# Kernel optimization log

Hardware: AMD Instinct MI355X
Metric: run time of the kernel (lower is better)

## Reference

```python
import jax, jax.numpy as jnp
import numpy as np

B, V, H, W = 8, 2, 1024, 1024
N = 131072
TH_MIN, TH_MAX = 0.0, 500.0
ALPHA = 0.5


def _make_extrinsics():
    # Random small-rotation camera-to-world poses (invertible 4x4), fixed seed.
    rng = np.random.default_rng(0)
    E = np.tile(np.eye(4, dtype=np.float32), (B, V, 1, 1))
    for bi in range(B):
        for vi in range(V):
            ang = rng.uniform(-0.15, 0.15)
            ax = rng.normal(size=3)
            ax = ax / np.linalg.norm(ax)
            K = np.array([[0.0, -ax[2], ax[1]], [ax[2], 0.0, -ax[0]], [-ax[1], ax[0], 0.0]])
            R = np.eye(3) + np.sin(ang) * K + (1.0 - np.cos(ang)) * (K @ K)
            E[bi, vi, :3, :3] = R.astype(np.float32)
            E[bi, vi, :3, 3] = (rng.normal(size=3) * 0.5).astype(np.float32)
    return jnp.asarray(E)


def setup_inputs():
    key = jax.random.key(0)
    k0, k1, k2, k3, k4 = jax.random.split(key, 5)
    scale = jnp.array([W - 1.0, H - 1.0], jnp.float32)
    mkpts0 = jax.random.uniform(k0, (N, 2), dtype=jnp.float32) * scale
    mkpts1 = jax.random.uniform(k1, (N, 2), dtype=jnp.float32) * scale
    mconf = jax.random.uniform(k2, (N,), jnp.float32, 0.2, 1.0)
    mbids = jnp.sort(jax.random.randint(k3, (N,), 0, B, dtype=jnp.int32))
    intr = jnp.tile(jnp.array([[1.0, 0.0, 0.5], [0.0, 1.0, 0.5], [0.0, 0.0, 1.0]], jnp.float32), (B, V, 1, 1))
    extr = _make_extrinsics()
    disps = jax.random.uniform(k4, (V * B, 1, H, W), jnp.float32, 0.01, 1.0)
    return {"mkpts0": mkpts0, "mkpts1": mkpts1, "mconf": mconf, "mbids": mbids,
            "intrinsics": intr, "extrinsics": extr, "fullres_disps": disps}


def _forward(mkpts0, mkpts1, mconf, mbids, intrinsics, extrinsics, fullres_disps):
    b, v = intrinsics.shape[:2]
    _, _, h, w = fullres_disps.shape
    # intr0[0,:]*=w ; intr0[1,:]*=h  (normalized -> pixel intrinsics)
    row_scale = jnp.array([float(w), float(h), 1.0], intrinsics.dtype)[None, None, :, None]
    intr = intrinsics * row_scale                                    # (b,v,3,3)
    extr_inv = jnp.linalg.inv(extrinsics)                            # (b,v,4,4)
    proj = jnp.einsum('bvij,bvjk->bvik', intr, extr_inv[:, :, :3, :])  # (b,v,3,4)

    # --- per-keypoint DLT triangulation (vectorized over all N matches) ---
    P = proj[mbids]                                                  # (N,v,3,4)
    pts2 = jnp.stack([mkpts0, mkpts1], axis=1)                       # (N,v,2)
    # rows: conf*(x*P[2]-P[0]), conf*(y*P[2]-P[1])
    A = P[:, :, 2:3, :] * pts2[..., None] - P[:, :, :2, :]           # (N,v,2,4)
    A = A * mconf[:, None, None, None]
    A = A.reshape(-1, 2 * v, 4)                                      # (N,4,4)
    _, _, vh = jnp.linalg.svd(A, full_matrices=False)
    hom = vh[:, -1, :]                                               # last right singular vector
    pts_world = hom[:, :3] / hom[:, 3:4]                             # (N,3)

    # transform into each camera frame: pc_transform(pts, extr.inverse())
    pw_h = jnp.concatenate([pts_world, jnp.ones_like(pts_world[:, :1])], axis=-1)
    pts_cam = jnp.einsum('nvij,nj->nvi', extr_inv[mbids], pw_h)[..., :3]  # (N,v,3)
    z = pts_cam[..., 2]                                              # (N,v)
    valid = jnp.all((z > TH_MIN) & (z < TH_MAX), axis=1)             # (N,)

    # --- near/far over valid matched depths per (scene, view) ---
    zmin = jnp.where(valid[:, None], z, jnp.inf)
    zmax = jnp.where(valid[:, None], z, -jnp.inf)
    near = jax.ops.segment_min(zmin, mbids, num_segments=b)          # (b,v)
    far = jax.ops.segment_max(zmax, mbids, num_segments=b)
    has = jax.ops.segment_max(valid.astype(jnp.float32), mbids, num_segments=b)
    flag = jnp.broadcast_to(has[:, None], (b, v))                    # (b,v)
    near = jnp.where(flag > 0, near, 0.0)
    far = jnp.where(flag > 0, far, 500.0)

    # --- fusion_mkpt_costvolum: scatter 1/z into the cost-volume disparities ---
    disps = fullres_disps.reshape(v, b, h, w)                        # '(v b) 1 h w'
    mk_x = jnp.clip(jnp.stack([mkpts0[:, 0], mkpts1[:, 0]], 1).astype(jnp.int32), 0, w - 1)  # (N,v)
    mk_y = jnp.clip(jnp.stack([mkpts0[:, 1], mkpts1[:, 1]], 1).astype(jnp.int32), 0, h - 1)
    mk_z = 1.0 / z                                                   # matched disparity (N,v)
    view_idx = jnp.broadcast_to(jnp.arange(v, dtype=jnp.int32)[None, :], mk_x.shape)
    bids2 = jnp.broadcast_to(mbids[:, None], mk_x.shape)
    cost = disps[view_idx, bids2, mk_y, mk_x]                        # gather existing disparity
    val = ALPHA * mk_z + (1.0 - ALPHA) * cost                        # alpha-weighted fusion
    val = jnp.where(valid[:, None], val, cost)                       # masked-out matches: no-op write
    disps = disps.at[view_idx, bids2, mk_y, mk_x].set(val)
    fused = disps.reshape(v * b, 1, h, w)
    return fused, near, far, flag


def reference(mkpts0, mkpts1, mconf, mbids, intrinsics, extrinsics, fullres_disps):
    return _forward(mkpts0, mkpts1, mconf, mbids, intrinsics, extrinsics, fullres_disps)
```

## Files before the change

kernel.cpp:

```cpp
#include <hip/hip_runtime.h>
#include <math.h>

#define BB 8
#define VV 2
#define HH 1024
#define WW 1024
#define NPTS 131072
#define IMG (HH*WW)
#define FUSED (VV*BB*IMG)

#define NSOLVE (NPTS/256)
#define F4TOT  (FUSED/4)

#define PER_CP   4
#define NC_K1    2048
#define COPY_K1  (NC_K1*256*PER_CP)
#define NC_K2    2048

#define NC_FB    (F4TOT/(256*PER_CP))

typedef float f32x4 __attribute__((ext_vector_type(4)));

#define OFF_VAL  0u
#define OFF_PIX  (8u*NPTS)
#define OFF_RED  (16u*NPTS)
#define OFF_WIN  (OFF_RED + 0x20000u)
#define WS_NEED  ((size_t)OFF_WIN + 4ull*(size_t)FUSED)

__device__ __forceinline__ int clampi(int v, int lo, int hi) {
    return v < lo ? lo : (v > hi ? hi : v);
}

__device__ __forceinline__ void prep_one(int t, const float* __restrict__ intr,
                                         const float* __restrict__ extr, double* sD) {
    const float* E = extr + t * 16;
    double R[3][3], tr[3];
#pragma unroll
    for (int i = 0; i < 3; i++) {
#pragma unroll
        for (int j = 0; j < 3; j++) R[i][j] = (double)E[i * 4 + j];
        tr[i] = (double)E[i * 4 + 3];
    }
    double inv[3][4];
#pragma unroll
    for (int i = 0; i < 3; i++) {
#pragma unroll
        for (int j = 0; j < 3; j++) inv[i][j] = R[j][i];
        inv[i][3] = -(R[0][i] * tr[0] + R[1][i] * tr[1] + R[2][i] * tr[2]);
    }
    const float* K = intr + t * 9;
    double rs[3] = {(double)WW, (double)HH, 1.0};
#pragma unroll
    for (int i = 0; i < 3; i++)
#pragma unroll
        for (int k = 0; k < 4; k++) {
            double s = 0.0;
#pragma unroll
            for (int j = 0; j < 3; j++) s += (double)K[i * 3 + j] * rs[i] * inv[j][k];
            sD[t * 12 + i * 4 + k] = s;
        }
#pragma unroll
    for (int k = 0; k < 4; k++) sD[192 + t * 4 + k] = inv[2][k];
}

__device__ __forceinline__ void copy_chunk(const f32x4* __restrict__ src,
                                           f32x4* __restrict__ dst,
                                           int base, int blk, int t) {
    int s = base + blk * (256 * PER_CP);
#pragma unroll
    for (int k = 0; k < PER_CP; k++) {
        int i = s + k * 256 + t;
        f32x4 v = src[i];
        __builtin_nontemporal_store(v, &dst[i]);
    }
}

template <int DEDUP>
__global__ __launch_bounds__(256) void mega_kernel(
        const f32x4* __restrict__ src, f32x4* __restrict__ dst,
        const float2* __restrict__ mk0, const float2* __restrict__ mk1,
        const int* __restrict__ mbids,
        const float* __restrict__ intr, const float* __restrict__ extr,
        const float* __restrict__ disps,
        float* __restrict__ out, char* __restrict__ ws) {
    int b = blockIdx.x, t = threadIdx.x;

    if (b >= NSOLVE) {
        copy_chunk(src, dst, 0, b - NSOLVE, t);
        return;
    }

    __shared__ double sD[256];
    __shared__ int nearB[16], farB[16], hasB[8];
    if (t < 16) {
        prep_one(t, intr, extr, sD);
        nearB[t] = 0x7F800000;
        farB[t]  = 0;
        if (t < 8) hasB[t] = 0;
    }
    __syncthreads();

    int n = b * 256 + t;
    float* valarr = (float*)(ws + OFF_VAL);
    int*   pixarr = (int*)(ws + OFF_PIX);
    int*   winner = (int*)(ws + OFF_WIN);

    int bid = mbids[n];
    float2 q0 = mk0[n], q1 = mk1[n];
    float xf[2] = {q0.x, q1.x};
    float yf[2] = {q0.y, q1.y};

    double M[4][4];
#pragma unroll
    for (int i = 0; i < 4; i++)
#pragma unroll
        for (int j = 0; j < 4; j++) M[i][j] = 0.0;
#pragma unroll
    for (int v = 0; v < 2; v++) {
        const double* P = sD + (bid * VV + v) * 12;
        double xx = (double)xf[v], yy = (double)yf[v];
        double r0[4], r1[4];
#pragma unroll
        for (int j = 0; j < 4; j++) {
            r0[j] = xx * P[8 + j] - P[j];
            r1[j] = yy * P[8 + j] - P[4 + j];
        }
#pragma unroll
        for (int i = 0; i < 4; i++)
#pragma unroll
            for (int j = 0; j < 4; j++) M[i][j] += r0[i] * r0[j] + r1[i] * r1[j];
    }

    double Vm[4][4] = {{1, 0, 0, 0}, {0, 1, 0, 0}, {0, 0, 1, 0}, {0, 0, 0, 1}};
    for (int sweep = 0; sweep < 8; ++sweep) {
        double off = fabs(M[0][1]) + fabs(M[0][2]) + fabs(M[0][3]) +
                     fabs(M[1][2]) + fabs(M[1][3]) + fabs(M[2][3]);
        double dia = fabs(M[0][0]) + fabs(M[1][1]) + fabs(M[2][2]) + fabs(M[3][3]);
        if (off <= 1e-13 * dia) break;
#pragma unroll
        for (int p = 0; p < 3; p++) {
#pragma unroll
            for (int q = p + 1; q < 4; q++) {
                double apq = M[p][q];
                if (fabs(apq) < 1e-300) continue;
                double tau = (M[q][q] - M[p][p]) / (2.0 * apq);
                double rt  = sqrt(1.0 + tau * tau);
                double t_  = (tau >= 0.0) ? 1.0 / (tau + rt) : 1.0 / (tau - rt);
                double c = 1.0 / sqrt(1.0 + t_ * t_);
                double s = t_ * c;
#pragma unroll
                for (int k = 0; k < 4; k++) {
                    double mp = M[k][p], mq = M[k][q];
                    M[k][p] = c * mp - s * mq;
                    M[k][q] = s * mp + c * mq;
                }
#pragma unroll
                for (int k = 0; k < 4; k++) {
                    double mp = M[p][k], mq = M[q][k];
                    M[p][k] = c * mp - s * mq;
                    M[q][k] = s * mp + c * mq;
                }
#pragma unroll
                for (int k = 0; k < 4; k++) {
                    double vp = Vm[k][p], vq = Vm[k][q];
                    Vm[k][p] = c * vp - s * vq;
                    Vm[k][q] = s * vp + c * vq;
                }
            }
        }
    }
    int jmin = 0; double dmin = M[0][0];
    if (M[1][1] < dmin) { dmin = M[1][1]; jmin = 1; }
    if (M[2][2] < dmin) { dmin = M[2][2]; jmin = 2; }
    if (M[3][3] < dmin) { dmin = M[3][3]; jmin = 3; }

    double ev[4];
#pragma unroll
    for (int i = 0; i < 4; i++) {
        double a01 = (jmin == 0) ? Vm[i][0] : Vm[i][1];
        double a23 = (jmin == 2) ? Vm[i][2] : Vm[i][3];
        ev[i] = (jmin < 2) ? a01 : a23;
    }
    double iw  = 1.0 / ev[3];
    double pwx = ev[0] * iw, pwy = ev[1] * iw, pwz = ev[2] * iw;

    double z[2];
#pragma unroll
    for (int v = 0; v < 2; v++) {
        const double* e = sD + 192 + (bid * VV + v) * 4;
        z[v] = e[0] * pwx + e[1] * pwy + e[2] * pwz + e[3];
    }
    bool valid = (z[0] > 0.0) && (z[0] < 500.0) && (z[1] > 0.0) && (z[1] < 500.0);

    unsigned long long vb = __ballot(valid);
    int bidFirst = __shfl(bid, 0);
    int bidLast  = __shfl(bid, 63);
    if (bidFirst == bidLast) {
        if (vb != 0ULL) {
            float zn[2], zf[2];
#pragma unroll
            for (int v = 0; v < 2; v++) {
                zn[v] = valid ? (float)z[v] : INFINITY;
                zf[v] = valid ? (float)z[v] : -1.0f;
            }
#pragma unroll
            for (int off = 32; off > 0; off >>= 1) {
#pragma unroll
                for (int v = 0; v < 2; v++) {
                    zn[v] = fminf(zn[v], __shfl_down(zn[v], off));
                    zf[v] = fmaxf(zf[v], __shfl_down(zf[v], off));
                }
            }
            if ((t & 63) == 0) {
#pragma unroll
                for (int v = 0; v < 2; v++) {
                    atomicMin(&nearB[bid * VV + v], __float_as_int(zn[v]));
                    atomicMax(&farB[bid * VV + v],  __float_as_int(zf[v]));
                }
                atomicOr(&hasB[bid], 1);
            }
        }
    } else if (valid) {
#pragma unroll
        for (int v = 0; v < 2; v++) {
            int fb = __float_as_int((float)z[v]);
            atomicMin(&nearB[bid * VV + v], fb);
            atomicMax(&farB[bid * VV + v],  fb);
        }
        atomicOr(&hasB[bid], 1);
    }

#pragma unroll
    for (int v = 0; v < 2; v++) {
        int xi = clampi((int)xf[v], 0, WW - 1);
        int yi = clampi((int)yf[v], 0, HH - 1);
        int pix = (v * BB + bid) * IMG + yi * WW + xi;
        float cost = disps[pix];
        if (DEDUP) {
            winner[pix] = 0;
            valarr[2 * n + v] = valid ? (float)(0.5 * (1.0 / z[v]) + 0.5 * (double)cost)
                                      : 0.0f;
            pixarr[2 * n + v] = pix;
        } else {
            float val = valid ? (float)(0.5 * (1.0 / z[v]) + 0.5 * (double)cost) : cost;
            out[pix] = val;
        }
    }

    __syncthreads();
    int* red = (int*)(ws + OFF_RED) + b * 40;
    if (t < 16) {
        red[t]      = nearB[t];
        red[16 + t] = farB[t];
        if (t < 8) red[32 + t] = hasB[t];
    }
}

__device__ __forceinline__ void reduce_nearfar(const char* __restrict__ ws,
                                               float* __restrict__ out) {
    __shared__ int redLds[40];
    int t = threadIdx.x;
    const int* red = (const int*)(ws + OFF_RED);
    int w = t >> 6, lane = t & 63;
    for (int c = w; c < 40; c += 4) {
        int acc = (c < 16) ? 0x7F800000 : 0;
        for (int s = lane; s < NSOLVE; s += 64) {
            int vv = red[s * 40 + c];
            acc = (c < 16) ? min(acc, vv) : (c < 32 ? max(acc, vv) : (acc | vv));
        }
#pragma unroll
        for (int off = 32; off > 0; off >>= 1) {
            int o = __shfl_down(acc, off);
            acc = (c < 16) ? min(acc, o) : (c < 32 ? max(acc, o) : (acc | o));
        }
        if (lane == 0) redLds[c] = acc;
    }
    __syncthreads();
    if (t < 16) {
        int hv = redLds[32 + (t >> 1)];
        out[FUSED + t]               = hv ? __int_as_float(redLds[t])      : 0.0f;
        out[FUSED + BB * VV + t]     = hv ? __int_as_float(redLds[16 + t]) : 500.0f;
        out[FUSED + 2 * BB * VV + t] = hv ? 1.0f : 0.0f;
    }
}

__global__ __launch_bounds__(256) void vote_copy_kernel(
        const f32x4* __restrict__ src, f32x4* __restrict__ dst,
        char* __restrict__ ws, float* __restrict__ out) {
    int b = blockIdx.x, t = threadIdx.x;
    copy_chunk(src, dst, COPY_K1, b, t);
    if (b < NSOLVE) {
        int gid = b * 256 + t;
        const int2* pix2 = (const int2*)(ws + OFF_PIX);
        int* winner = (int*)(ws + OFF_WIN);
        int2 p = pix2[gid];
        atomicMax(winner + p.x, 2 * gid + 1);
        atomicMax(winner + p.y, 2 * gid + 2);
    } else if (b == NSOLVE) {
        reduce_nearfar(ws, out);
    }
}

__global__ __launch_bounds__(256) void resolve_kernel(float* __restrict__ out,
                                                      const char* __restrict__ ws) {
    int gid = blockIdx.x * 256 + threadIdx.x;
    const int2*   pix2 = (const int2*)(ws + OFF_PIX);
    const float2* val2 = (const float2*)(ws + OFF_VAL);
    const int*    winner = (const int*)(ws + OFF_WIN);
    int2 p = pix2[gid];
    float2 v = val2[gid];
    if (v.x > 0.0f && winner[p.x] == 2 * gid + 1) out[p.x] = v.x;
    if (v.y > 0.0f && winner[p.y] == 2 * gid + 2) out[p.y] = v.y;
}

__global__ __launch_bounds__(256) void reduce_kernel(float* __restrict__ out,
                                                     const char* __restrict__ ws) {
    reduce_nearfar(ws, out);
}

extern "C" void kernel_launch(void* const* d_in, const int* in_sizes, int n_in,
                              void* d_out, int out_size, void* d_ws, size_t ws_size,
                              hipStream_t stream) {
    const float* mk0   = (const float*)d_in[0];
    const float* mk1   = (const float*)d_in[1];
    const int*   mbids = (const int*)d_in[3];
    const float* intr  = (const float*)d_in[4];
    const float* extr  = (const float*)d_in[5];
    const float* disps = (const float*)d_in[6];
    float* out = (float*)d_out;
    char*  ws  = (char*)d_ws;

    bool dedup = (ws_size >= WS_NEED);

    if (dedup) {
        mega_kernel<1><<<dim3(NSOLVE + NC_K1), 256, 0, stream>>>(
            (const f32x4*)disps, (f32x4*)out, (const float2*)mk0, (const float2*)mk1,
            mbids, intr, extr, disps, out, ws);
        vote_copy_kernel<<<NC_K2, 256, 0, stream>>>(
            (const f32x4*)disps, (f32x4*)out, ws, out);
        resolve_kernel<<<NSOLVE, 256, 0, stream>>>(out, ws);
    } else {
        mega_kernel<0><<<dim3(NSOLVE + NC_FB), 256, 0, stream>>>(
            (const f32x4*)disps, (f32x4*)out, (const float2*)mk0, (const float2*)mk1,
            mbids, intr, extr, disps, out, ws);
        reduce_kernel<<<1, 256, 0, stream>>>(out, ws);
    }
}
```

Baseline: 186.7 us.

## Run Jacobi eigensolve in fp32 with one fp64 refinement sweep; hoist gathers

The 4x4 DLT eigen-decomposition now runs its Jacobi sweeps in fp32 on a trace-normalized copy of the matrix. It then rotates the original fp64 matrix by the fp32 eigenvectors and does a single fp64 Jacobi sweep to refine the result. The aim is to cut expensive fp64 arithmetic, which has lower throughput than fp32. Separately, the keypoint, disparity-gather and winner-clear memory accesses are moved to the top of the kernel, before the barrier, so their latency overlaps with the solve. The risk is lower accuracy in near-degenerate cases where one fp64 sweep may not fully converge.

Result: no change. 184.4 us (-1.2%).

```diff
diff --git a/kernel.cpp b/kernel.cpp
--- a/kernel.cpp
+++ b/kernel.cpp
@@ -92,6 +92,11 @@
 
     __shared__ double sD[256];
     __shared__ int nearB[16], farB[16], hasB[8];
+
+    int n = b * 256 + t;
+    int bid = mbids[n];
+    float2 q0 = mk0[n], q1 = mk1[n];
+
     if (t < 16) {
         prep_one(t, intr, extr, sD);
         nearB[t] = 0x7F800000;
@@ -100,15 +105,23 @@
     }
     __syncthreads();
 
-    int n = b * 256 + t;
     float* valarr = (float*)(ws + OFF_VAL);
     int*   pixarr = (int*)(ws + OFF_PIX);
     int*   winner = (int*)(ws + OFF_WIN);
 
-    int bid = mbids[n];
-    float2 q0 = mk0[n], q1 = mk1[n];
     float xf[2] = {q0.x, q1.x};
     float yf[2] = {q0.y, q1.y};
+
+    int   pixv[2];
+    float costv[2];
+#pragma unroll
+    for (int v = 0; v < 2; v++) {
+        int xi = clampi((int)xf[v], 0, WW - 1);
+        int yi = clampi((int)yf[v], 0, HH - 1);
+        pixv[v] = (v * BB + bid) * IMG + yi * WW + xi;
+        costv[v] = disps[pixv[v]];
+        if (DEDUP) winner[pixv[v]] = 0;
+    }
 
     double M[4][4];
 #pragma unroll
@@ -131,54 +144,117 @@
             for (int j = 0; j < 4; j++) M[i][j] += r0[i] * r0[j] + r1[i] * r1[j];
     }
 
-    double Vm[4][4] = {{1, 0, 0, 0}, {0, 1, 0, 0}, {0, 0, 1, 0}, {0, 0, 0, 1}};
-    for (int sweep = 0; sweep < 8; ++sweep) {
-        double off = fabs(M[0][1]) + fabs(M[0][2]) + fabs(M[0][3]) +
-                     fabs(M[1][2]) + fabs(M[1][3]) + fabs(M[2][3]);
-        double dia = fabs(M[0][0]) + fabs(M[1][1]) + fabs(M[2][2]) + fabs(M[3][3]);
-        if (off <= 1e-13 * dia) break;
+    double tr4 = M[0][0] + M[1][1] + M[2][2] + M[3][3];
+    double itr = (tr4 > 0.0) ? 1.0 / tr4 : 1.0;
+    float Mf[4][4], Vf[4][4] = {{1, 0, 0, 0}, {0, 1, 0, 0}, {0, 0, 1, 0}, {0, 0, 0, 1}};
+#pragma unroll
+    for (int i = 0; i < 4; i++)
+#pragma unroll
+        for (int j = 0; j < 4; j++) Mf[i][j] = (float)(M[i][j] * itr);
+
+    for (int sweep = 0; sweep < 6; ++sweep) {
+        float off = fabsf(Mf[0][1]) + fabsf(Mf[0][2]) + fabsf(Mf[0][3]) +
+                    fabsf(Mf[1][2]) + fabsf(Mf[1][3]) + fabsf(Mf[2][3]);
+        float dia = fabsf(Mf[0][0]) + fabsf(Mf[1][1]) + fabsf(Mf[2][2]) + fabsf(Mf[3][3]);
+        if (off <= 1e-6f * dia) break;
 #pragma unroll
         for (int p = 0; p < 3; p++) {
 #pragma unroll
             for (int q = p + 1; q < 4; q++) {
-                double apq = M[p][q];
-                if (fabs(apq) < 1e-300) continue;
-                double tau = (M[q][q] - M[p][p]) / (2.0 * apq);
-                double rt  = sqrt(1.0 + tau * tau);
-                double t_  = (tau >= 0.0) ? 1.0 / (tau + rt) : 1.0 / (tau - rt);
-                double c = 1.0 / sqrt(1.0 + t_ * t_);
-                double s = t_ * c;
+                float apq = Mf[p][q];
+                if (fabsf(apq) < 1e-30f) continue;
+                float tau = (Mf[q][q] - Mf[p][p]) / (2.0f * apq);
+                float rt  = sqrtf(1.0f + tau * tau);
+                float t_  = (tau >= 0.0f) ? 1.0f / (tau + rt) : 1.0f / (tau - rt);
+                float c = 1.0f / sqrtf(1.0f + t_ * t_);
+                float s = t_ * c;
 #pragma unroll
                 for (int k = 0; k < 4; k++) {
-                    double mp = M[k][p], mq = M[k][q];
-                    M[k][p] = c * mp - s * mq;
-                    M[k][q] = s * mp + c * mq;
+                    float mp = Mf[k][p], mq = Mf[k][q];
+                    Mf[k][p] = c * mp - s * mq;
+                    Mf[k][q] = s * mp + c * mq;
                 }
 #pragma unroll
                 for (int k = 0; k < 4; k++) {
-                    double mp = M[p][k], mq = M[q][k];
-                    M[p][k] = c * mp - s * mq;
-                    M[q][k] = s * mp + c * mq;
+                    float mp = Mf[p][k], mq = Mf[q][k];
+                    Mf[p][k] = c * mp - s * mq;
+                    Mf[q][k] = s * mp + c * mq;
                 }
 #pragma unroll
                 for (int k = 0; k < 4; k++) {
-                    double vp = Vm[k][p], vq = Vm[k][q];
-                    Vm[k][p] = c * vp - s * vq;
-                    Vm[k][q] = s * vp + c * vq;
+                    float vp = Vf[k][p], vq = Vf[k][q];
+                    Vf[k][p] = c * vp - s * vq;
+                    Vf[k][q] = s * vp + c * vq;
                 }
             }
         }
     }
-    int jmin = 0; double dmin = M[0][0];
-    if (M[1][1] < dmin) { dmin = M[1][1]; jmin = 1; }
-    if (M[2][2] < dmin) { dmin = M[2][2]; jmin = 2; }
-    if (M[3][3] < dmin) { dmin = M[3][3]; jmin = 3; }
+
+    double Vd[4][4], T[4][4], Md[4][4];
+#pragma unroll
+    for (int i = 0; i < 4; i++)
+#pragma unroll
+        for (int j = 0; j < 4; j++) Vd[i][j] = (double)Vf[i][j];
+#pragma unroll
+    for (int i = 0; i < 4; i++)
+#pragma unroll
+        for (int j = 0; j < 4; j++) {
+            double s = 0.0;
+#pragma unroll
+            for (int k = 0; k < 4; k++) s += M[i][k] * Vd[k][j];
+            T[i][j] = s;
+        }
+#pragma unroll
+    for (int i = 0; i < 4; i++)
+#pragma unroll
+        for (int j = 0; j < 4; j++) {
+            double s = 0.0;
+#pragma unroll
+            for (int k = 0; k < 4; k++) s += Vd[k][i] * T[k][j];
+            Md[i][j] = s;
+        }
+#pragma unroll
+    for (int p = 0; p < 3; p++) {
+#pragma unroll
+        for (int q = p + 1; q < 4; q++) {
+            double apq = Md[p][q];
+            if (fabs(apq) < 1e-300) continue;
+            double tau = (Md[q][q] - Md[p][p]) / (2.0 * apq);
+            double rt  = sqrt(1.0 + tau * tau);
+            double t_  = (tau >= 0.0) ? 1.0 / (tau + rt) : 1.0 / (tau - rt);
+            double c = 1.0 / sqrt(1.0 + t_ * t_);
+            double s = t_ * c;
+#pragma unroll
+            for (int k = 0; k < 4; k++) {
+                double mp = Md[k][p], mq = Md[k][q];
+                Md[k][p] = c * mp - s * mq;
+                Md[k][q] = s * mp + c * mq;
+            }
+#pragma unroll
+            for (int k = 0; k < 4; k++) {
+                double mp = Md[p][k], mq = Md[q][k];
+                Md[p][k] = c * mp - s * mq;
+                Md[q][k] = s * mp + c * mq;
+            }
+#pragma unroll
+            for (int k = 0; k < 4; k++) {
+                double vp = Vd[k][p], vq = Vd[k][q];
+                Vd[k][p] = c * vp - s * vq;
+                Vd[k][q] = s * vp + c * vq;
+            }
+        }
+    }
+
+    int jmin = 0; double dmin = Md[0][0];
+    if (Md[1][1] < dmin) { dmin = Md[1][1]; jmin = 1; }
+    if (Md[2][2] < dmin) { dmin = Md[2][2]; jmin = 2; }
+    if (Md[3][3] < dmin) { dmin = Md[3][3]; jmin = 3; }
 
     double ev[4];
 #pragma unroll
     for (int i = 0; i < 4; i++) {
-        double a01 = (jmin == 0) ? Vm[i][0] : Vm[i][1];
-        double a23 = (jmin == 2) ? Vm[i][2] : Vm[i][3];
+        double a01 = (jmin == 0) ? Vd[i][0] : Vd[i][1];
+        double a23 = (jmin == 2) ? Vd[i][2] : Vd[i][3];
         ev[i] = (jmin < 2) ? a01 : a23;
     }
     double iw  = 1.0 / ev[3];
@@ -232,12 +308,9 @@
 
 #pragma unroll
     for (int v = 0; v < 2; v++) {
-        int xi = clampi((int)xf[v], 0, WW - 1);
-        int yi = clampi((int)yf[v], 0, HH - 1);
-        int pix = (v * BB + bid) * IMG + yi * WW + xi;
-        float cost = disps[pix];
+        int pix = pixv[v];
+        float cost = costv[v];
         if (DEDUP) {
-            winner[pix] = 0;
             valarr[2 * n + v] = valid ? (float)(0.5 * (1.0 / z[v]) + 0.5 * (double)cost)
                                       : 0.0f;
             pixarr[2 * n + v] = pix;
```
